# Performance work log

Hardware: AMD Instinct MI355X
Metric: run time of the kernel (lower is better)

The kernel has to match this reference:

```python
import math
import jax, jax.numpy as jnp
import numpy as np

B = 1024
D = 384
Q = 65536
TOPK = 128
HARD_W = 2.0
TEMP_START = 0.2
TEMP_END = 0.05
WARMUP = 10


def _temperature(epoch):
    # curriculum cosine decay (epoch is a Python int)
    if epoch >= WARMUP:
        return TEMP_END
    progress = epoch / max(1, WARMUP)
    return TEMP_END + 0.5 * (TEMP_START - TEMP_END) * (1.0 + math.cos(math.pi * progress))


def _normalize(x):
    # F.normalize: x / max(||x||, eps)
    n = jnp.linalg.norm(x, axis=-1, keepdims=True)
    return x / jnp.maximum(n, 1e-12)


def _hard_neg_reweight(logits):
    # logits: [B, N]; labels = arange(B) (diagonal positives)
    b = logits.shape[0]
    rows = jnp.arange(b)
    neg_logits = logits.at[rows, rows].set(-jnp.inf)      # mask positives
    _, hard_idx = jax.lax.top_k(neg_logits, TOPK)          # [B, TOPK] hardest negatives
    weights = jnp.ones_like(logits)
    weights = weights.at[rows[:, None], hard_idx].set(HARD_W)
    weights = weights.at[rows, rows].set(1.0)
    return logits * weights


def _cross_entropy_diag(logits):
    b = logits.shape[0]
    logp = jax.nn.log_softmax(logits, axis=-1)
    return -jnp.mean(logp[jnp.arange(b), jnp.arange(b)])


def setup_inputs() -> dict:
    key = jax.random.key(0)
    k1, k2, k3, k4 = jax.random.split(key, 4)
    rgb_feat = jax.random.normal(k1, (B, D), dtype=jnp.float32)
    ir_feat = jax.random.normal(k2, (B, D), dtype=jnp.float32)
    rgb_queue = _normalize(jax.random.normal(k3, (Q, D), dtype=jnp.float32))
    ir_queue = _normalize(jax.random.normal(k4, (Q, D), dtype=jnp.float32))
    return {"rgb_feat": rgb_feat, "ir_feat": ir_feat,
            "rgb_queue": rgb_queue, "ir_queue": ir_queue, "epoch": 0}


def reference(rgb_feat, ir_feat, rgb_queue, ir_queue, epoch):
    temp = _temperature(epoch)
    rgb_z = _normalize(rgb_feat.astype(jnp.float32))
    ir_z = _normalize(ir_feat.astype(jnp.float32))
    ir_all = jnp.concatenate([ir_z, ir_queue], axis=0)    # [B+Q, D]
    rgb_all = jnp.concatenate([rgb_z, rgb_queue], axis=0)
    logits_r2i = (rgb_z @ ir_all.T) / temp                # [B, B+Q]
    logits_i2r = (ir_z @ rgb_all.T) / temp
    logits_r2i = _hard_neg_reweight(logits_r2i)
    logits_i2r = _hard_neg_reweight(logits_i2r)
    return 0.5 * (_cross_entropy_diag(logits_r2i) + _cross_entropy_diag(logits_i2r))
```

## Files before the change

kernel.cpp:

```cpp
#include <hip/hip_runtime.h>
#include <hip/hip_bf16.h>

#define B_    1024
#define D_    384
#define Q_    65536
#define N_    66560
#define TOPK_ 128

#define NBIN_ 4096
#define CAP_  2048

typedef __bf16 bf16x8 __attribute__((ext_vector_type(8)));
typedef float  f32x4  __attribute__((ext_vector_type(4)));
typedef unsigned short u16;
typedef u16 u16x8 __attribute__((ext_vector_type(8)));

__device__ __forceinline__ unsigned short f2bf(float x) {
  unsigned int u = __float_as_uint(x);
  unsigned int r = (u + 0x7fffu + ((u >> 16) & 1u)) >> 16;
  return (unsigned short)r;
}

__device__ __forceinline__ void gld_lds16(const void* g, void* l) {
  __builtin_amdgcn_global_load_lds(
      (__attribute__((address_space(1))) void*)(g),
      (__attribute__((address_space(3))) void*)(l), 16, 0, 0);
}

__device__ __forceinline__ void wait_vmcnt(int n) {
  switch (n) {
    case 12: asm volatile("s_waitcnt vmcnt(12)" ::: "memory"); break;
    case 8:  asm volatile("s_waitcnt vmcnt(8)"  ::: "memory"); break;
    case 4:  asm volatile("s_waitcnt vmcnt(4)"  ::: "memory"); break;
    default: asm volatile("s_waitcnt vmcnt(0)"  ::: "memory"); break;
  }
}

__device__ __forceinline__ unsigned int bf2key(unsigned int u) {
  return u ^ ((u & 0x8000u) ? 0xFFFFu : 0x8000u);
}

__global__ __launch_bounds__(64) void k_normalize(
    const float* __restrict__ rgb, const float* __restrict__ ir,
    const int* __restrict__ ep,
    u16* __restrict__ zrA, u16* __restrict__ ziA,
    u16* __restrict__ zrU, u16* __restrict__ ziU)
{
  int r = blockIdx.x & (B_ - 1);
  bool isIr = blockIdx.x >= B_;
  const float* src = (isIr ? ir : rgb) + (size_t)r * D_;
  u16* dA = (isIr ? ziA : zrA) + (size_t)r * D_;
  u16* dU = (isIr ? ziU : zrU) + (size_t)r * D_;
  int t = threadIdx.x;
  float x[6]; float ss = 0.f;
  #pragma unroll
  for (int k = 0; k < 6; ++k) { x[k] = src[t + 64*k]; ss += x[k]*x[k]; }
  #pragma unroll
  for (int off = 32; off > 0; off >>= 1) ss += __shfl_down(ss, off);
  ss = __shfl(ss, 0);
  float inv = 1.0f / fmaxf(sqrtf(ss), 1e-12f);

  int e = ep[0];
  float temp;
  if (e >= 10) temp = 0.05f;
  else {
    float p = (float)e * 0.1f;
    temp = 0.05f + 0.075f * (1.0f + cosf(3.14159265358979323846f * p));
  }
  float itemp = 1.0f / temp;

  #pragma unroll
  for (int k = 0; k < 6; ++k) {
    float z = x[k] * inv;
    dU[t + 64*k] = f2bf(z);
    dA[t + 64*k] = f2bf(z * itemp);
  }
}

__global__ __launch_bounds__(256) void k_build_ball(
    const u16* __restrict__ zU, const float* __restrict__ queue,
    u16* __restrict__ ball)
{
  size_t i = ((size_t)blockIdx.x * 256 + threadIdx.x) * 8;
  const size_t zElems = (size_t)B_ * D_;
  if (i < zElems) {
    *(uint4*)(ball + i) = *(const uint4*)(zU + i);
  } else {
    const float* q = queue + (i - zElems);
    float4 a = *(const float4*)q;
    float4 b = *(const float4*)(q + 4);
    u16x8 o;
    o[0] = f2bf(a.x); o[1] = f2bf(a.y); o[2] = f2bf(a.z); o[3] = f2bf(a.w);
    o[4] = f2bf(b.x); o[5] = f2bf(b.y); o[6] = f2bf(b.z); o[7] = f2bf(b.w);
    *(u16x8*)(ball + i) = o;
  }
}

#define BK_ 32
#define NSTEP_ 12
__global__ __launch_bounds__(256, 2) void k_gemm(
    const u16* __restrict__ A,
    const u16* __restrict__ ball,
    u16* __restrict__ C,
    float* __restrict__ diag,
    int r0, int mtiles)
{
  __shared__ __align__(16) unsigned char smem[65536];
  u16* Ct = (u16*)smem;

  int bid = blockIdx.x;
  int nwg = gridDim.x;
  int cpx = nwg >> 3;
  int wgid = (bid & 7) * cpx + (bid >> 3);
  int nt = wgid / mtiles;
  int mt = wgid - nt * mtiles;

  const int tid  = threadIdx.x;
  const int wave = tid >> 6, lane = tid & 63;
  const int wm = wave >> 1, wn = wave & 1;
  const int mbase = mt * 128;
  const int nbase = nt * 128;
  const u16* Ab = A    + (size_t)(r0 + mbase) * D_;
  const u16* Bb = ball + (size_t)nbase * D_;

  auto As = [&](int t) -> u16* { return (u16*)(smem + (t & 3) * 8192); };
  auto Bs = [&](int t) -> u16* { return (u16*)(smem + 32768 + (t & 3) * 8192); };
  auto stage = [&](int t) {
    const int ks = t * BK_;
    #pragma unroll
    for (int i = 0; i < 2; ++i) {
      int f = i * 256 + tid;
      int rr = f >> 2, cc = f & 3;
      int koff = (((cc * 16) ^ (((rr >> 1) & 3) << 4)) >> 1);
      gld_lds16(Ab + (size_t)rr * D_ + ks + koff, As(t) + (size_t)f * 8);
      gld_lds16(Bb + (size_t)rr * D_ + ks + koff, Bs(t) + (size_t)f * 8);
    }
  };

  f32x4 acc[4][4];
  #pragma unroll
  for (int m = 0; m < 4; ++m)
    #pragma unroll
    for (int n = 0; n < 4; ++n)
      #pragma unroll
      for (int r = 0; r < 4; ++r) acc[m][n][r] = 0.0f;

  const int lr = lane & 15;
  const int kb = (lane >> 4) * 16;

  stage(0); stage(1); stage(2);

  #pragma unroll
  for (int t = 0; t < NSTEP_; ++t) {
    if (t + 3 < NSTEP_) stage(t + 3);
    wait_vmcnt(t < NSTEP_ - 3 ? 12 : (NSTEP_ - 1 - t) * 4);
    __builtin_amdgcn_s_barrier();
    __builtin_amdgcn_sched_barrier(0);

    const u16* Ac = As(t);
    const u16* Bc = Bs(t);
    bf16x8 af[4], bq[4];
    #pragma unroll
    for (int m = 0; m < 4; ++m) {
      int row = wm*64 + m*16 + lr;
      af[m] = *(const bf16x8*)((const char*)Ac + row * 64 + (kb ^ (((row >> 1) & 3) << 4)));
    }
    #pragma unroll
    for (int n = 0; n < 4; ++n) {
      int row = wn*64 + n*16 + lr;
      bq[n] = *(const bf16x8*)((const char*)Bc + row * 64 + (kb ^ (((row >> 1) & 3) << 4)));
    }
    #pragma unroll
    for (int m = 0; m < 4; ++m)
      #pragma unroll
      for (int n = 0; n < 4; ++n)
        acc[m][n] = __builtin_amdgcn_mfma_f32_16x16x32_bf16(af[m], bq[n], acc[m][n], 0, 0, 0);

    asm volatile("s_waitcnt lgkmcnt(0)" ::: "memory");
    __builtin_amdgcn_sched_barrier(0);
    __builtin_amdgcn_s_barrier();
  }

  const int rowq = (lane >> 4) * 4;
  #pragma unroll
  for (int m = 0; m < 4; ++m) {
    #pragma unroll
    for (int n = 0; n < 4; ++n) {
      int lcol = wn*64 + n*16 + lr;
      int gcol = nbase + lcol;
      #pragma unroll
      for (int r = 0; r < 4; ++r) {
        int lrow = wm*64 + m*16 + rowq + r;
        float x = acc[m][n][r];
        int grow = r0 + mbase + lrow;
        if (gcol == grow) { diag[grow] = x; x = -60.0f; }
        Ct[lrow * 136 + lcol] = f2bf(x);
      }
    }
  }
  __syncthreads();

  int rrow = tid >> 4;
  int cchunk = (tid & 15) * 8;
  #pragma unroll
  for (int pass = 0; pass < 8; ++pass) {
    int row = pass * 16 + rrow;
    u16x8 v = *(const u16x8*)(Ct + row * 136 + cchunk);
    *(u16x8*)(C + (size_t)(mbase + row) * N_ + nbase + cchunk) = v;
  }
}

__global__ __launch_bounds__(256) void k_select(
    const u16* __restrict__ C, const float* __restrict__ diag,
    float* __restrict__ rowloss, int r0)
{
  __shared__ unsigned int hist[NBIN_];
  __shared__ float vals[CAP_];
  __shared__ float fred[256];
  __shared__ unsigned int csum[256];
  __shared__ int sh_bstar, sh_above, sh_cnt;

  const int t = threadIdx.x;
  const int grow = r0 + blockIdx.x;
  const u16x8* p = (const u16x8*)(C + (size_t)blockIdx.x * N_);

  uint4* h4 = (uint4*)hist;
  #pragma unroll
  for (int i = 0; i < 4; ++i) h4[i * 256 + t] = make_uint4(0,0,0,0);
  if (t == 0) sh_cnt = 0;
  __syncthreads();

  float es0 = 0.f, es1 = 0.f;
  #pragma unroll 1
  for (int base = 0; base < 8192; base += 2048) {
    u16x8 v[8];
    #pragma unroll
    for (int j = 0; j < 8; ++j) v[j] = p[base + j * 256 + t];
    #pragma unroll
    for (int j = 0; j < 8; ++j) {
      #pragma unroll
      for (int e = 0; e < 8; ++e) {
        unsigned int u = (unsigned int)(unsigned short)v[j][e];
        atomicAdd(&hist[bf2key(u) >> 4], 1u);
        float ex = __expf(__uint_as_float(u << 16));
        if (j & 1) es1 += ex; else es0 += ex;
      }
    }
  }
  if (t < 128) {
    u16x8 v = p[8192 + t];
    #pragma unroll
    for (int e = 0; e < 8; ++e) {
      unsigned int u = (unsigned int)(unsigned short)v[e];
      atomicAdd(&hist[bf2key(u) >> 4], 1u);
      es0 += __expf(__uint_as_float(u << 16));
    }
  }
  float esum = es0 + es1;
  __syncthreads();

  unsigned int S = 0;
  #pragma unroll
  for (int i = 0; i < 16; ++i) S += hist[t * 16 + i];
  csum[t] = S;
  __syncthreads();

  unsigned int a = S;
  #pragma unroll
  for (int s = 1; s < 256; s <<= 1) {
    unsigned int add = (t + s < 256) ? csum[t + s] : 0u;
    __syncthreads();
    a += add; csum[t] = a;
    __syncthreads();
  }

  int above_chunk = (t < 255) ? (int)csum[t + 1] : 0;
  if (above_chunk < TOPK_ && above_chunk + (int)S >= TOPK_) {
    int cum = above_chunk;
    #pragma unroll 1
    for (int i = 15; i >= 0; --i) {
      int c = (int)hist[t * 16 + i];
      if (cum + c >= TOPK_) { sh_bstar = t * 16 + i; sh_above = cum; break; }
      cum += c;
    }
  }
  __syncthreads();
  const unsigned int bstar = (unsigned int)sh_bstar;
  const int A = sh_above;

  float delta = 0.f;
  #pragma unroll 1
  for (int base = 0; base < 8192; base += 2048) {
    u16x8 v[8];
    #pragma unroll
    for (int j = 0; j < 8; ++j) v[j] = p[base + j * 256 + t];
    #pragma unroll
    for (int j = 0; j < 8; ++j) {
      #pragma unroll
      for (int e = 0; e < 8; ++e) {
        unsigned int u = (unsigned int)(unsigned short)v[j][e];
        unsigned int bin = bf2key(u) >> 4;
        if (bin >= bstar) {
          float val = __uint_as_float(u << 16);
          if (bin > bstar) delta += __expf(2.f * val) - __expf(val);
          else { int s = atomicAdd(&sh_cnt, 1); if (s < CAP_) vals[s] = val; }
        }
      }
    }
  }
  if (t < 128) {
    u16x8 v = p[8192 + t];
    #pragma unroll
    for (int e = 0; e < 8; ++e) {
      unsigned int u = (unsigned int)(unsigned short)v[e];
      unsigned int bin = bf2key(u) >> 4;
      if (bin >= bstar) {
        float val = __uint_as_float(u << 16);
        if (bin > bstar) delta += __expf(2.f * val) - __expf(val);
        else { int s = atomicAdd(&sh_cnt, 1); if (s < CAP_) vals[s] = val; }
      }
    }
  }
  __syncthreads();

  int C2 = sh_cnt < CAP_ ? sh_cnt : CAP_;
  int need = TOPK_ - A;
  for (int i = t; i < C2; i += 256) {
    float v = vals[i];
    int g = 0;
    for (int k = 0; k < C2; ++k)
      g += (vals[k] > v) || (vals[k] == v && k < i);
    if (g < need) delta += __expf(2.f * v) - __expf(v);
  }

  fred[t] = esum + delta;
  __syncthreads();
  #pragma unroll
  for (int s = 128; s > 0; s >>= 1) { if (t < s) fred[t] += fred[t + s]; __syncthreads(); }

  if (t == 0) {
    float d = diag[grow];
    rowloss[grow] = logf(fred[0] + __expf(d)) - d;
  }
}

__global__ __launch_bounds__(256) void k_final(
    const float* __restrict__ rowloss, float* __restrict__ out)
{
  __shared__ float red[256];
  int t = threadIdx.x;
  float s = 0.f;
  for (int i = t; i < 2 * B_; i += 256) s += rowloss[i];
  red[t] = s;
  __syncthreads();
  for (int k = 128; k > 0; k >>= 1) { if (t < k) red[t] += red[t + k]; __syncthreads(); }
  if (t == 0) out[0] = red[0] * (1.0f / (2.0f * B_));
}

extern "C" void kernel_launch(void* const* d_in, const int* in_sizes, int n_in,
                              void* d_out, int out_size, void* d_ws, size_t ws_size,
                              hipStream_t stream)
{
  const float* rgb_feat = (const float*)d_in[0];
  const float* ir_feat  = (const float*)d_in[1];
  const float* rgb_q    = (const float*)d_in[2];
  const float* ir_q     = (const float*)d_in[3];
  const int*   epoch    = (const int*)d_in[4];

  char* ws = (char*)d_ws;
  size_t off = 0;
  auto alloc = [&](size_t bytes) -> char* {
    char* p = ws + off;
    off = (off + bytes + 255) & ~(size_t)255;
    return p;
  };

  u16* zrA = (u16*)alloc((size_t)B_ * D_ * 2);
  u16* ziA = (u16*)alloc((size_t)B_ * D_ * 2);
  u16* zrU = (u16*)alloc((size_t)B_ * D_ * 2);
  u16* ziU = (u16*)alloc((size_t)B_ * D_ * 2);
  float* diag    = (float*)alloc((size_t)2 * B_ * 4);
  float* rowloss = (float*)alloc((size_t)2 * B_ * 4);
  u16* ball = (u16*)alloc((size_t)N_ * D_ * 2);

  size_t avail = ws_size > off ? ws_size - off : 0;
  int SR = (int)(avail / ((size_t)N_ * 2));
  SR &= ~127;
  if (SR > B_) SR = B_;
  if (SR < 128) SR = 128;
  u16* slab = (u16*)(ws + off);

  k_normalize<<<dim3(2 * B_), dim3(64), 0, stream>>>(
      rgb_feat, ir_feat, epoch, zrA, ziA, zrU, ziU);

  for (int dir = 0; dir < 2; ++dir) {
    const u16*   Amat   = (dir == 0) ? zrA : ziA;
    const u16*   zOther = (dir == 0) ? ziU : zrU;
    const float* queue  = (dir == 0) ? ir_q : rgb_q;
    float* diagD = diag    + dir * B_;
    float* lossD = rowloss + dir * B_;

    k_build_ball<<<dim3((unsigned)((size_t)N_ * D_ / 8 / 256)), dim3(256), 0, stream>>>(
        zOther, queue, ball);

    for (int r0 = 0; r0 < B_; r0 += SR) {
      int cur = (B_ - r0) < SR ? (B_ - r0) : SR;
      int mtiles = cur / 128;
      int nwg = (N_ / 128) * mtiles;
      k_gemm<<<dim3(nwg), dim3(256), 0, stream>>>(
          Amat, ball, slab, diagD, r0, mtiles);
      k_select<<<dim3(cur), dim3(256), 0, stream>>>(slab, diagD, lossD, r0);
    }
  }

  k_final<<<dim3(1), dim3(256), 0, stream>>>(rowloss, (float*)d_out);
}
```

Before: 318.1 us.

## Enlarge GEMM tile to 256x256 with 512-thread blocks and triple buffering

The logits GEMM moves from 128x128 tiles with 4 waves to 256x256 tiles with 8 waves, each wave computing a 128x64 sub-tile. LDS staging changes from quad buffering of small K-slices to triple buffering of 32KB stages. The XCD-aware block remap now handles grid sizes not divisible by 8, and the epilogue writes the tile out in two 128-row halves through LDS. The larger tile is meant to raise operand reuse and cut global/LDS traffic per FLOP, at the cost of more registers, 96KB of shared memory, fewer workgroups and a shallower prefetch pipeline.

```diff
diff --git a/kernel.cpp b/kernel.cpp
--- a/kernel.cpp
+++ b/kernel.cpp
@@ -29,7 +29,6 @@
 
 __device__ __forceinline__ void wait_vmcnt(int n) {
   switch (n) {
-    case 12: asm volatile("s_waitcnt vmcnt(12)" ::: "memory"); break;
     case 8:  asm volatile("s_waitcnt vmcnt(8)"  ::: "memory"); break;
     case 4:  asm volatile("s_waitcnt vmcnt(4)"  ::: "memory"); break;
     default: asm volatile("s_waitcnt vmcnt(0)"  ::: "memory"); break;
@@ -98,38 +97,38 @@
 
 #define BK_ 32
 #define NSTEP_ 12
-__global__ __launch_bounds__(256, 2) void k_gemm(
+__global__ __launch_bounds__(512, 2) void k_gemm(
     const u16* __restrict__ A,
     const u16* __restrict__ ball,
     u16* __restrict__ C,
     float* __restrict__ diag,
     int r0, int mtiles)
 {
-  __shared__ __align__(16) unsigned char smem[65536];
+  __shared__ __align__(16) unsigned char smem[98304];
   u16* Ct = (u16*)smem;
 
-  int bid = blockIdx.x;
-  int nwg = gridDim.x;
-  int cpx = nwg >> 3;
-  int wgid = (bid & 7) * cpx + (bid >> 3);
+  int bid = blockIdx.x, nwg = gridDim.x;
+  int xcd = bid & 7, loc = bid >> 3;
+  int q = nwg >> 3, rr8 = nwg & 7;
+  int wgid = (xcd < rr8 ? xcd * (q + 1) : rr8 * (q + 1) + (xcd - rr8) * q) + loc;
   int nt = wgid / mtiles;
   int mt = wgid - nt * mtiles;
 
   const int tid  = threadIdx.x;
   const int wave = tid >> 6, lane = tid & 63;
-  const int wm = wave >> 1, wn = wave & 1;
-  const int mbase = mt * 128;
-  const int nbase = nt * 128;
+  const int wm = wave >> 2, wn = wave & 3;
+  const int mbase = mt * 256;
+  const int nbase = nt * 256;
   const u16* Ab = A    + (size_t)(r0 + mbase) * D_;
   const u16* Bb = ball + (size_t)nbase * D_;
 
-  auto As = [&](int t) -> u16* { return (u16*)(smem + (t & 3) * 8192); };
-  auto Bs = [&](int t) -> u16* { return (u16*)(smem + 32768 + (t & 3) * 8192); };
+  auto As = [&](int t) -> u16* { return (u16*)(smem + (t % 3) * 32768); };
+  auto Bs = [&](int t) -> u16* { return (u16*)(smem + (t % 3) * 32768 + 16384); };
   auto stage = [&](int t) {
     const int ks = t * BK_;
     #pragma unroll
     for (int i = 0; i < 2; ++i) {
-      int f = i * 256 + tid;
+      int f = i * 512 + tid;
       int rr = f >> 2, cc = f & 3;
       int koff = (((cc * 16) ^ (((rr >> 1) & 3) << 4)) >> 1);
       gld_lds16(Ab + (size_t)rr * D_ + ks + koff, As(t) + (size_t)f * 8);
@@ -137,9 +136,9 @@
     }
   };
 
-  f32x4 acc[4][4];
-  #pragma unroll
-  for (int m = 0; m < 4; ++m)
+  f32x4 acc[8][4];
+  #pragma unroll
+  for (int m = 0; m < 8; ++m)
     #pragma unroll
     for (int n = 0; n < 4; ++n)
       #pragma unroll
@@ -148,21 +147,21 @@
   const int lr = lane & 15;
   const int kb = (lane >> 4) * 16;
 
-  stage(0); stage(1); stage(2);
+  stage(0); stage(1);
 
   #pragma unroll
   for (int t = 0; t < NSTEP_; ++t) {
-    if (t + 3 < NSTEP_) stage(t + 3);
-    wait_vmcnt(t < NSTEP_ - 3 ? 12 : (NSTEP_ - 1 - t) * 4);
+    if (t + 2 < NSTEP_) stage(t + 2);
+    wait_vmcnt(t < NSTEP_ - 2 ? 8 : (t == NSTEP_ - 2 ? 4 : 0));
     __builtin_amdgcn_s_barrier();
     __builtin_amdgcn_sched_barrier(0);
 
     const u16* Ac = As(t);
     const u16* Bc = Bs(t);
-    bf16x8 af[4], bq[4];
-    #pragma unroll
-    for (int m = 0; m < 4; ++m) {
-      int row = wm*64 + m*16 + lr;
+    bf16x8 af[8], bq[4];
+    #pragma unroll
+    for (int m = 0; m < 8; ++m) {
+      int row = wm*128 + m*16 + lr;
       af[m] = *(const bf16x8*)((const char*)Ac + row * 64 + (kb ^ (((row >> 1) & 3) << 4)));
     }
     #pragma unroll
@@ -171,7 +170,7 @@
       bq[n] = *(const bf16x8*)((const char*)Bc + row * 64 + (kb ^ (((row >> 1) & 3) << 4)));
     }
     #pragma unroll
-    for (int m = 0; m < 4; ++m)
+    for (int m = 0; m < 8; ++m)
       #pragma unroll
       for (int n = 0; n < 4; ++n)
         acc[m][n] = __builtin_amdgcn_mfma_f32_16x16x32_bf16(af[m], bq[n], acc[m][n], 0, 0, 0);
@@ -183,30 +182,34 @@
 
   const int rowq = (lane >> 4) * 4;
   #pragma unroll
-  for (int m = 0; m < 4; ++m) {
-    #pragma unroll
-    for (int n = 0; n < 4; ++n) {
-      int lcol = wn*64 + n*16 + lr;
-      int gcol = nbase + lcol;
+  for (int pass = 0; pass < 2; ++pass) {
+    if (pass) __syncthreads();
+    if (wm == pass) {
       #pragma unroll
-      for (int r = 0; r < 4; ++r) {
-        int lrow = wm*64 + m*16 + rowq + r;
-        float x = acc[m][n][r];
-        int grow = r0 + mbase + lrow;
-        if (gcol == grow) { diag[grow] = x; x = -60.0f; }
-        Ct[lrow * 136 + lcol] = f2bf(x);
+      for (int m = 0; m < 8; ++m) {
+        #pragma unroll
+        for (int n = 0; n < 4; ++n) {
+          int lcol = wn*64 + n*16 + lr;
+          int gcol = nbase + lcol;
+          #pragma unroll
+          for (int r = 0; r < 4; ++r) {
+            int lrow = m*16 + rowq + r;
+            float x = acc[m][n][r];
+            int grow = r0 + mbase + pass*128 + lrow;
+            if (gcol == grow) { diag[grow] = x; x = -60.0f; }
+            Ct[lrow * 264 + lcol] = f2bf(x);
+          }
+        }
       }
     }
-  }
-  __syncthreads();
-
-  int rrow = tid >> 4;
-  int cchunk = (tid & 15) * 8;
-  #pragma unroll
-  for (int pass = 0; pass < 8; ++pass) {
-    int row = pass * 16 + rrow;
-    u16x8 v = *(const u16x8*)(Ct + row * 136 + cchunk);
-    *(u16x8*)(C + (size_t)(mbase + row) * N_ + nbase + cchunk) = v;
+    __syncthreads();
+    #pragma unroll
+    for (int j = 0; j < 8; ++j) {
+      int id = j * 512 + tid;
+      int row = id >> 5, cc8 = (id & 31) * 8;
+      u16x8 v = *(const u16x8*)(Ct + row * 264 + cc8);
+      *(u16x8*)(C + (size_t)(mbase + pass*128 + row) * N_ + nbase + cc8) = v;
+    }
   }
 }
 
@@ -385,9 +388,9 @@
 
   size_t avail = ws_size > off ? ws_size - off : 0;
   int SR = (int)(avail / ((size_t)N_ * 2));
-  SR &= ~127;
+  SR &= ~255;
   if (SR > B_) SR = B_;
-  if (SR < 128) SR = 128;
+  if (SR < 256) SR = 256;
   u16* slab = (u16*)(ws + off);
 
   k_normalize<<<dim3(2 * B_), dim3(64), 0, stream>>>(
@@ -405,9 +408,9 @@
 
     for (int r0 = 0; r0 < B_; r0 += SR) {
       int cur = (B_ - r0) < SR ? (B_ - r0) : SR;
-      int mtiles = cur / 128;
-      int nwg = (N_ / 128) * mtiles;
-      k_gemm<<<dim3(nwg), dim3(256), 0, stream>>>(
+      int mtiles = cur / 256;
+      int nwg = (N_ / 256) * mtiles;
+      k_gemm<<<dim3(nwg), dim3(512), 0, stream>>>(
           Amat, ball, slab, diagD, r0, mtiles);
       k_select<<<dim3(cur), dim3(256), 0, stream>>>(slab, diagD, lossD, r0);
     }
```

Result: slower. 394.2 us (+23.9%).
